# Kernel optimization log

Measured on AMD Instinct MI355X. Metric: run time of the kernel, lower is better.

The kernel has to match this reference:

```python
import jax, jax.numpy as jnp
import numpy as np

N_HEAD = 16


def setup_inputs() -> dict:
    key = jax.random.key(0)
    k1, k2, k3 = jax.random.split(key, 3)
    B, T, C = 4, 2048, 2048
    x = jax.random.normal(k1, (B, T, C), dtype=jnp.float32)
    # weights stored as [in, out] so y = x @ W + b (equivalent to torch Linear)
    w_attn = jax.random.normal(k2, (C, 3 * C), dtype=jnp.float32) * 0.02
    b_attn = jnp.zeros((3 * C,), dtype=jnp.float32)
    w_proj = jax.random.normal(k3, (C, C), dtype=jnp.float32) * 0.02
    b_proj = jnp.zeros((C,), dtype=jnp.float32)
    return {"x": x, "w_attn": w_attn, "b_attn": b_attn, "w_proj": w_proj, "b_proj": b_proj}


def reference(x, w_attn, b_attn, w_proj, b_proj):
    B, T, C = x.shape
    H = N_HEAD
    D = C // H
    qkv = x @ w_attn + b_attn                     # [B,T,3C]
    q, k, v = jnp.split(qkv, 3, axis=-1)
    q = q.reshape(B, T, H, D).transpose(0, 2, 1, 3)  # [B,H,T,D]
    k = k.reshape(B, T, H, D).transpose(0, 2, 1, 3)
    v = v.reshape(B, T, H, D).transpose(0, 2, 1, 3)
    att = jnp.einsum("bhqd,bhkd->bhqk", q, k) * (1.0 / jnp.sqrt(jnp.float32(D)))
    causal = jnp.tril(jnp.ones((T, T), dtype=bool))
    att = jnp.where(causal[None, None], att, jnp.float32(-jnp.inf))
    att = jax.nn.softmax(att, axis=-1)
    y = jnp.einsum("bhqk,bhkd->bhqd", att, v)     # [B,H,T,D]
    y = y.transpose(0, 2, 1, 3).reshape(B, T, C)
    return y @ w_proj + b_proj
```

## Files before the change

kernel.cpp:

```cpp
#include <hip/hip_runtime.h>
#include <cstdint>

typedef unsigned short u16;
typedef u16   u16x4 __attribute__((ext_vector_type(4)));
typedef u16   u16x8 __attribute__((ext_vector_type(8)));
typedef short s16x8 __attribute__((ext_vector_type(8)));
typedef float f32x4 __attribute__((ext_vector_type(4)));

__device__ __forceinline__ u16 f2bf(float f) {
  union { float f; unsigned u; } v; v.f = f;
  unsigned u = v.u;
  return (u16)((u + 0x7fffu + ((u >> 16) & 1u)) >> 16);
}

__device__ __forceinline__ void gld_lds16(const u16* g, u16* l) {
  __builtin_amdgcn_global_load_lds((const __attribute__((address_space(1))) void*)g,
                                   (__attribute__((address_space(3))) void*)l, 16, 0, 0);
}

__device__ __forceinline__ void transpose_cast_body(
    const float* __restrict__ in, u16* __restrict__ outp, int R, int Cin,
    int cx, int cy, u16 (*tile)[72]) {
  const int c0 = cx * 64, r0 = cy * 64;
  const int t = threadIdx.x;
  const int r = t >> 2, cs = (t & 3) * 16;
  const float* src = in + (size_t)(r0 + r) * Cin + c0 + cs;
#pragma unroll
  for (int q = 0; q < 4; ++q) {
    float4 v = *(const float4*)(src + q * 4);
    tile[r][cs + q * 4 + 0] = f2bf(v.x);
    tile[r][cs + q * 4 + 1] = f2bf(v.y);
    tile[r][cs + q * 4 + 2] = f2bf(v.z);
    tile[r][cs + q * 4 + 3] = f2bf(v.w);
  }
  __syncthreads();
  u16x8 w0, w1;
#pragma unroll
  for (int q = 0; q < 8; ++q) { w0[q] = tile[cs + q][r]; w1[q] = tile[cs + 8 + q][r]; }
  u16* dst = outp + (size_t)(c0 + r) * R + r0 + cs;
  *(u16x8*)dst = w0;
  *(u16x8*)(dst + 8) = w1;
}

__global__ void prep_k(const float* __restrict__ x, u16* __restrict__ xb,
                       const float* __restrict__ w_attn, u16* __restrict__ waT,
                       const float* __restrict__ w_proj, u16* __restrict__ wpT) {
  __shared__ u16 tile[64][72];
  const int bx = blockIdx.x;
  if (bx < 8192) {
    size_t i = ((size_t)bx * 256 + threadIdx.x) * 8;
    float4 a = *(const float4*)(x + i);
    float4 b = *(const float4*)(x + i + 4);
    u16x8 r;
    r[0] = f2bf(a.x); r[1] = f2bf(a.y); r[2] = f2bf(a.z); r[3] = f2bf(a.w);
    r[4] = f2bf(b.x); r[5] = f2bf(b.y); r[6] = f2bf(b.z); r[7] = f2bf(b.w);
    *(u16x8*)(xb + i) = r;
  } else if (bx < 11264) {
    int idx = bx - 8192;
    transpose_cast_body(w_attn, waT, 2048, 6144, idx % 96, idx / 96, tile);
  } else {
    int idx = bx - 11264;
    transpose_cast_body(w_proj, wpT, 2048, 2048, idx % 32, idx / 32, tile);
  }
}

template <int EPI>
__global__ __launch_bounds__(512, 2) void gemm256(
    const u16* __restrict__ A, const u16* __restrict__ Bt,
    const float* __restrict__ bias,
    u16* __restrict__ o0, u16* __restrict__ o1, u16* __restrict__ o2,
    float* __restrict__ ofp, int Ntiles, int Kdim) {
  __shared__ __align__(128) u16 sm[65536];
  const int nwg = gridDim.x;
  const int orig = blockIdx.x;
  const int qq = nwg >> 3;
  const int bid = (orig & 7) * qq + (orig >> 3);
  const int mt = bid / Ntiles, nt = bid % Ntiles;
  const int tid = threadIdx.x, lane = tid & 63, wave = tid >> 6;
  const int wr = wave >> 2, wc = wave & 3;
  const int l15 = lane & 15, lhi = lane >> 4;
  const int r7 = l15 & 7, r3 = l15 >> 3;
  f32x4 acc[8][4] = {};
  const int nK = Kdim >> 6;

#define VMA(n) asm volatile("s_waitcnt vmcnt(" #n ")" ::: "memory")
#define BARK   asm volatile("s_barrier" ::: "memory")
#define DSA(qm)                                                                          \
  do {                                                                                   \
    _Pragma("unroll") for (int mi = 0; mi < 4; ++mi)                                     \
    _Pragma("unroll") for (int kk = 0; kk < 2; ++kk)                                     \
      af[mi * 2 + kk] = *(const s16x8*)&sm[(size_t)(cA + (qm) * 1024 +                   \
          (wr * 8 + mi * 2 + r3) * 64 + r7 * 8 + (((kk) * 4 + lhi) ^ r7)) * 8];          \
  } while (0)
#define DSB(dst, qn)                                                                     \
  do {                                                                                   \
    _Pragma("unroll") for (int ni = 0; ni < 2; ++ni)                                     \
    _Pragma("unroll") for (int kk = 0; kk < 2; ++kk)                                     \
      dst[ni * 2 + kk] = *(const s16x8*)&sm[(size_t)(cB + (qn) * 1024 +                  \
          (wc * 4 + ni * 2 + r3) * 64 + r7 * 8 + (((kk) * 4 + lhi) ^ r7)) * 8];          \
  } while (0)
#define STA(unit, k0, sbase)                                                             \
  do {                                                                                   \
    _Pragma("unroll") for (int l = 0; l < 2; ++l) {                                      \
      int c = l * 512 + tid;                                                             \
      int mid = (c >> 3) & 7;                                                            \
      int rowL = (c >> 6) * 8 + mid, khi = (c & 7) ^ mid;                                \
      int prow = (rowL >> 6) * 128 + (unit) * 64 + (rowL & 63);                          \
      gld_lds16(A + (size_t)(mt * 256 + prow) * Kdim + (k0) + khi * 8,                   \
                &sm[(size_t)((sbase) + (unit)*1024 + l * 512 + wave * 64) * 8]);         \
    }                                                                                    \
  } while (0)
#define STB(unit, k0, sbase)                                                             \
  do {                                                                                   \
    _Pragma("unroll") for (int l = 0; l < 2; ++l) {                                      \
      int c = l * 512 + tid;                                                             \
      int mid = (c >> 3) & 7;                                                            \
      int colL = (c >> 6) * 8 + mid, khi = (c & 7) ^ mid;                                \
      int pcol = (colL >> 5) * 64 + (unit) * 32 + (colL & 31);                           \
      gld_lds16(Bt + (size_t)(nt * 256 + pcol) * Kdim + (k0) + khi * 8,                  \
                &sm[(size_t)((sbase) + (unit)*1024 + l * 512 + wave * 64) * 8]);         \
    }                                                                                    \
  } while (0)
#define MM(qm, qn, BF)                                                                   \
  do {                                                                                   \
    __builtin_amdgcn_s_setprio(1);                                                       \
    _Pragma("unroll") for (int mi = 0; mi < 4; ++mi)                                     \
    _Pragma("unroll") for (int ni = 0; ni < 2; ++ni)                                     \
    _Pragma("unroll") for (int kk = 0; kk < 2; ++kk)                                     \
      acc[(qm) * 4 + mi][(qn) * 2 + ni] = __builtin_amdgcn_mfma_f32_16x16x32_bf16(       \
          af[mi * 2 + kk], BF[ni * 2 + kk], acc[(qm) * 4 + mi][(qn) * 2 + ni], 0, 0, 0); \
    __builtin_amdgcn_s_setprio(0);                                                       \
  } while (0)

  STA(0, 0, 0); STB(0, 0, 4096); STB(1, 0, 4096); STA(1, 0, 0);
  VMA(4);
  BARK;

  for (int t = 0; t < nK; ++t) {
    const int cA = (t & 1) * 2048, cB = 4096 + (t & 1) * 2048;
    const int sA = ((t & 1) ^ 1) * 2048, sB = 4096 + ((t & 1) ^ 1) * 2048;
    const int k1 = (t + 1) << 6;
    const bool st = (t + 1 < nK);
    s16x8 af[8], bf0[4], bf1[4];
    DSA(0); DSB(bf0, 0);
    if (st) { STA(0, k1, sA); VMA(4); } else { VMA(2); }
    BARK; MM(0, 0, bf0); BARK;
    DSB(bf1, 1);
    if (st) { STB(0, k1, sB); VMA(4); } else { VMA(0); }
    BARK; MM(0, 1, bf1); BARK;
    DSA(1);
    if (st) STB(1, k1, sB);
    BARK; MM(1, 1, bf1); BARK;
    if (st) { STA(1, k1, sA); VMA(4); }
    BARK; MM(1, 0, bf0); BARK;
  }
#undef VMA
#undef BARK
#undef DSA
#undef DSB
#undef STA
#undef STB
#undef MM

  const int row0 = mt * 256 + wr * 128;
  const int col0 = nt * 256 + wc * 64;
  float bcol[4];
#pragma unroll
  for (int ni = 0; ni < 4; ++ni) bcol[ni] = bias[col0 + ni * 16 + l15];
  if constexpr (EPI == 0) {
#pragma unroll
    for (int ni = 0; ni < 4; ++ni) {
      int cc = col0 + ni * 16 + l15;
      int which = cc >> 11, h = (cc >> 7) & 15, d = cc & 127;
      if (which == 2) {
#pragma unroll
        for (int mi = 0; mi < 8; ++mi) {
          int t0 = row0 + mi * 16 + lhi * 4;
          int bb = t0 >> 11, tt = t0 & 2047;
          u16x4 w;
#pragma unroll
          for (int j = 0; j < 4; ++j) w[j] = f2bf(acc[mi][ni][j] + bcol[ni]);
          *(u16x4*)&o2[(((size_t)bb * 16 + h) * 128 + d) * 2048 + tt] = w;
        }
      } else {
        u16* o = (which == 0) ? o0 : o1;
#pragma unroll
        for (int mi = 0; mi < 8; ++mi)
#pragma unroll
          for (int j = 0; j < 4; ++j) {
            int row = row0 + mi * 16 + lhi * 4 + j;
            int bb = row >> 11, tt = row & 2047;
            o[(((size_t)bb * 16 + h) * 2048 + tt) * 128 + d] = f2bf(acc[mi][ni][j] + bcol[ni]);
          }
      }
    }
  } else {
#pragma unroll
    for (int mi = 0; mi < 8; ++mi)
#pragma unroll
      for (int j = 0; j < 4; ++j) {
        int row = row0 + mi * 16 + lhi * 4 + j;
#pragma unroll
        for (int ni = 0; ni < 4; ++ni)
          ofp[(size_t)row * 2048 + col0 + ni * 16 + l15] = acc[mi][ni][j] + bcol[ni];
      }
  }
}

__global__ __launch_bounds__(512, 4) void attn_k(
    const u16* __restrict__ Q, const u16* __restrict__ Kg,
    const u16* __restrict__ Vt, u16* __restrict__ Y) {
  __shared__ u16 Ks[8192];
  __shared__ u16 Vs[8192];
  __shared__ u16 Ps[8][16 * 72];
  const int p = blockIdx.x, bh = blockIdx.y;
  const int tid = threadIdx.x, lane = tid & 63, wave = tid >> 6;
  const int l15 = lane & 15, lhi = lane >> 4;
  const size_t bhT = (size_t)bh * 2048;
  const int b = bh >> 4, h = bh & 15;
  const float sc = 0.08838834764831845f * 1.4426950408889634f;

  for (int hf = 0; hf < 2; ++hf) {
    const int qt = hf ? 15 - p : p;
    const int r0 = qt * 128 + wave * 16;
    const int last = 2 * qt + 1;

    s16x8 qf[4];
#pragma unroll
    for (int kk = 0; kk < 4; ++kk)
      qf[kk] = *(const s16x8*)&Q[(bhT + r0 + l15) * 128 + kk * 32 + lhi * 8];

    f32x4 o[8] = {};
    float m_[4], l_[4];
#pragma unroll
    for (int j = 0; j < 4; ++j) { m_[j] = -1e30f; l_[j] = 0.f; }

    __syncthreads();
#pragma unroll
    for (int c = 0; c < 2; ++c) {
      int ci = c * 512 + tid;
      int dhi = ci >> 6, key = ci & 63;
      gld_lds16(Kg + (bhT + key) * 128 + dhi * 8, &Ks[(c * 512 + wave * 64) * 8]);
      int khi = ci >> 7, d = ci & 127;
      gld_lds16(Vt + ((size_t)bh * 128 + d) * 2048 + khi * 8, &Vs[(c * 512 + wave * 64) * 8]);
    }
    __syncthreads();

    for (int it = 0; it <= last; ++it) {
      const int j0 = it * 64;
      const bool have_next = (it < last);
      u16x8 kpre[2], vpre[2];
      if (have_next) {
        const int j1 = j0 + 64;
#pragma unroll
        for (int c = 0; c < 2; ++c) {
          int ci = c * 512 + tid;
          int dhi = ci >> 6, key = ci & 63;
          kpre[c] = *(const u16x8*)&Kg[(bhT + j1 + key) * 128 + dhi * 8];
          int khi = ci >> 7, d = ci & 127;
          vpre[c] = *(const u16x8*)&Vt[((size_t)bh * 128 + d) * 2048 + j1 + khi * 8];
        }
      }

      if (j0 <= r0 + 15) {
        f32x4 s[4] = {};
        __builtin_amdgcn_s_setprio(1);
#pragma unroll
        for (int nc = 0; nc < 4; ++nc)
#pragma unroll
          for (int kk = 0; kk < 4; ++kk) {
            s16x8 kf = *(const s16x8*)&Ks[((kk * 4 + lhi) * 64 + nc * 16 + l15) * 8];
            s[nc] = __builtin_amdgcn_mfma_f32_16x16x32_bf16(qf[kk], kf, s[nc], 0, 0, 0);
          }
        __builtin_amdgcn_s_setprio(0);
        const bool maskt = (j0 + 63 > r0);
        float rmax[4];
#pragma unroll
        for (int j = 0; j < 4; ++j) rmax[j] = -1e30f;
#pragma unroll
        for (int nc = 0; nc < 4; ++nc)
#pragma unroll
          for (int j = 0; j < 4; ++j) {
            float v = s[nc][j] * sc;
            if (maskt && (j0 + nc * 16 + l15) > (r0 + lhi * 4 + j)) v = -1e30f;
            s[nc][j] = v;
            rmax[j] = fmaxf(rmax[j], v);
          }
#pragma unroll
        for (int off = 1; off < 16; off <<= 1)
#pragma unroll
          for (int j = 0; j < 4; ++j) rmax[j] = fmaxf(rmax[j], __shfl_xor(rmax[j], off));

        bool up = false;
#pragma unroll
        for (int j = 0; j < 4; ++j) up |= (rmax[j] > m_[j] + 8.f);
        if (__any(up)) {
#pragma unroll
          for (int j = 0; j < 4; ++j) {
            float mn = fmaxf(m_[j], rmax[j]);
            float al = exp2f(m_[j] - mn);
            m_[j] = mn;
            l_[j] *= al;
#pragma unroll
            for (int di = 0; di < 8; ++di) o[di][j] *= al;
          }
        }
        float rsum[4];
#pragma unroll
        for (int j = 0; j < 4; ++j) rsum[j] = 0.f;
#pragma unroll
        for (int nc = 0; nc < 4; ++nc)
#pragma unroll
          for (int j = 0; j < 4; ++j) {
            float pv = exp2f(s[nc][j] - m_[j]);
            rsum[j] += pv;
            Ps[wave][(lhi * 4 + j) * 72 + nc * 16 + l15] = f2bf(pv);
          }
#pragma unroll
        for (int off = 1; off < 16; off <<= 1)
#pragma unroll
          for (int j = 0; j < 4; ++j) rsum[j] += __shfl_xor(rsum[j], off);
#pragma unroll
        for (int j = 0; j < 4; ++j) l_[j] += rsum[j];

        __builtin_amdgcn_s_setprio(1);
#pragma unroll
        for (int kk2 = 0; kk2 < 2; ++kk2) {
          s16x8 pf = *(const s16x8*)&Ps[wave][l15 * 72 + kk2 * 32 + lhi * 8];
#pragma unroll
          for (int di = 0; di < 8; ++di) {
            s16x8 vf = *(const s16x8*)&Vs[((kk2 * 4 + lhi) * 128 + di * 16 + l15) * 8];
            o[di] = __builtin_amdgcn_mfma_f32_16x16x32_bf16(pf, vf, o[di], 0, 0, 0);
          }
        }
        __builtin_amdgcn_s_setprio(0);
      }

      if (have_next) {
        __syncthreads();
#pragma unroll
        for (int c = 0; c < 2; ++c) {
          *(u16x8*)&Ks[(c * 512 + tid) * 8] = kpre[c];
          *(u16x8*)&Vs[(c * 512 + tid) * 8] = vpre[c];
        }
        __syncthreads();
      }
    }

    float rl[4];
#pragma unroll
    for (int j = 0; j < 4; ++j) rl[j] = 1.0f / l_[j];
#pragma unroll
    for (int di = 0; di < 8; ++di)
#pragma unroll
      for (int j = 0; j < 4; ++j) {
        int row = b * 2048 + r0 + lhi * 4 + j;
        int col = h * 128 + di * 16 + l15;
        Y[(size_t)row * 2048 + col] = f2bf(o[di][j] * rl[j]);
      }
  }
}

extern "C" void kernel_launch(void* const* d_in, const int* in_sizes, int n_in,
                              void* d_out, int out_size, void* d_ws, size_t ws_size,
                              hipStream_t stream) {
  const float* x      = (const float*)d_in[0];
  const float* w_attn = (const float*)d_in[1];
  const float* b_attn = (const float*)d_in[2];
  const float* w_proj = (const float*)d_in[3];
  const float* b_proj = (const float*)d_in[4];
  float* out = (float*)d_out;

  char* ws = (char*)d_ws;
  u16* xb  = (u16*)(ws);
  u16* waT = (u16*)(ws + 33554432ull);
  u16* wpT = (u16*)(ws + 58720256ull);
  u16* Qb  = (u16*)(ws + 67108864ull);
  u16* Kb  = (u16*)(ws + 100663296ull);
  u16* Vtb = (u16*)(ws + 167772160ull);
  u16* Yb  = xb;

  prep_k<<<12288, 256, 0, stream>>>(x, xb, w_attn, waT, w_proj, wpT);
  gemm256<0><<<32 * 24, 512, 0, stream>>>(xb, waT, b_attn, Qb, Kb, Vtb, nullptr, 24, 2048);
  attn_k<<<dim3(8, 64), 512, 0, stream>>>(Qb, Kb, Vtb, Yb);
  gemm256<1><<<32 * 8, 512, 0, stream>>>(Yb, wpT, b_proj, nullptr, nullptr, nullptr, out, 8, 2048);
}
```

Measured before the change: 487.2 us.

## Double-buffer attention K/V tiles in LDS with async global-to-LDS loads

The attention kernel now keeps two LDS buffers for K and V. Each iteration issues direct global-to-LDS loads for the next tile into the spare buffer while computing on the current one. This replaces the register prefetch and its two barriers plus LDS stores with a single barrier per iteration, and aims to hide load latency and cut register pressure. The grid axes are also swapped so head/batch varies fastest, which changes block scheduling order. In exchange, LDS use per block roughly doubles for K/V, which may lower the number of resident blocks per CU.

After: 525.6 us. +7.9%, slower.

```diff
diff --git a/kernel.cpp b/kernel.cpp
--- a/kernel.cpp
+++ b/kernel.cpp
@@ -210,16 +210,30 @@
 __global__ __launch_bounds__(512, 4) void attn_k(
     const u16* __restrict__ Q, const u16* __restrict__ Kg,
     const u16* __restrict__ Vt, u16* __restrict__ Y) {
-  __shared__ u16 Ks[8192];
-  __shared__ u16 Vs[8192];
+  __shared__ u16 Ks[2][8192];
+  __shared__ u16 Vs[2][8192];
   __shared__ u16 Ps[8][16 * 72];
-  const int p = blockIdx.x, bh = blockIdx.y;
+  const int bh = blockIdx.x, p = blockIdx.y;
   const int tid = threadIdx.x, lane = tid & 63, wave = tid >> 6;
   const int l15 = lane & 15, lhi = lane >> 4;
   const size_t bhT = (size_t)bh * 2048;
   const int b = bh >> 4, h = bh & 15;
   const float sc = 0.08838834764831845f * 1.4426950408889634f;
 
+#define STAGEKV(buf, jt)                                                   \
+  do {                                                                     \
+    const int jb_ = (jt) * 64;                                             \
+    _Pragma("unroll") for (int c = 0; c < 2; ++c) {                        \
+      int ci = c * 512 + tid;                                              \
+      int dhi = ci >> 6, key = ci & 63;                                    \
+      gld_lds16(Kg + (bhT + jb_ + key) * 128 + dhi * 8,                    \
+                &Ks[buf][(c * 512 + wave * 64) * 8]);                      \
+      int khi = ci >> 7, d = ci & 127;                                     \
+      gld_lds16(Vt + ((size_t)bh * 128 + d) * 2048 + jb_ + khi * 8,        \
+                &Vs[buf][(c * 512 + wave * 64) * 8]);                      \
+    }                                                                      \
+  } while (0)
+
   for (int hf = 0; hf < 2; ++hf) {
     const int qt = hf ? 15 - p : p;
     const int r0 = qt * 128 + wave * 16;
@@ -236,31 +250,13 @@
     for (int j = 0; j < 4; ++j) { m_[j] = -1e30f; l_[j] = 0.f; }
 
     __syncthreads();
-#pragma unroll
-    for (int c = 0; c < 2; ++c) {
-      int ci = c * 512 + tid;
-      int dhi = ci >> 6, key = ci & 63;
-      gld_lds16(Kg + (bhT + key) * 128 + dhi * 8, &Ks[(c * 512 + wave * 64) * 8]);
-      int khi = ci >> 7, d = ci & 127;
-      gld_lds16(Vt + ((size_t)bh * 128 + d) * 2048 + khi * 8, &Vs[(c * 512 + wave * 64) * 8]);
-    }
-    __syncthreads();
+    STAGEKV(0, 0);
 
     for (int it = 0; it <= last; ++it) {
       const int j0 = it * 64;
-      const bool have_next = (it < last);
-      u16x8 kpre[2], vpre[2];
-      if (have_next) {
-        const int j1 = j0 + 64;
-#pragma unroll
-        for (int c = 0; c < 2; ++c) {
-          int ci = c * 512 + tid;
-          int dhi = ci >> 6, key = ci & 63;
-          kpre[c] = *(const u16x8*)&Kg[(bhT + j1 + key) * 128 + dhi * 8];
-          int khi = ci >> 7, d = ci & 127;
-          vpre[c] = *(const u16x8*)&Vt[((size_t)bh * 128 + d) * 2048 + j1 + khi * 8];
-        }
-      }
+      const int buf = it & 1;
+      __syncthreads();
+      if (it < last) STAGEKV(buf ^ 1, it + 1);
 
       if (j0 <= r0 + 15) {
         f32x4 s[4] = {};
@@ -269,7 +265,7 @@
         for (int nc = 0; nc < 4; ++nc)
 #pragma unroll
           for (int kk = 0; kk < 4; ++kk) {
-            s16x8 kf = *(const s16x8*)&Ks[((kk * 4 + lhi) * 64 + nc * 16 + l15) * 8];
+            s16x8 kf = *(const s16x8*)&Ks[buf][((kk * 4 + lhi) * 64 + nc * 16 + l15) * 8];
             s[nc] = __builtin_amdgcn_mfma_f32_16x16x32_bf16(qf[kk], kf, s[nc], 0, 0, 0);
           }
         __builtin_amdgcn_s_setprio(0);
@@ -329,21 +325,11 @@
           s16x8 pf = *(const s16x8*)&Ps[wave][l15 * 72 + kk2 * 32 + lhi * 8];
 #pragma unroll
           for (int di = 0; di < 8; ++di) {
-            s16x8 vf = *(const s16x8*)&Vs[((kk2 * 4 + lhi) * 128 + di * 16 + l15) * 8];
+            s16x8 vf = *(const s16x8*)&Vs[buf][((kk2 * 4 + lhi) * 128 + di * 16 + l15) * 8];
             o[di] = __builtin_amdgcn_mfma_f32_16x16x32_bf16(pf, vf, o[di], 0, 0, 0);
           }
         }
         __builtin_amdgcn_s_setprio(0);
-      }
-
-      if (have_next) {
-        __syncthreads();
-#pragma unroll
-        for (int c = 0; c < 2; ++c) {
-          *(u16x8*)&Ks[(c * 512 + tid) * 8] = kpre[c];
-          *(u16x8*)&Vs[(c * 512 + tid) * 8] = vpre[c];
-        }
-        __syncthreads();
       }
     }
 
@@ -359,6 +345,7 @@
         Y[(size_t)row * 2048 + col] = f2bf(o[di][j] * rl[j]);
       }
   }
+#undef STAGEKV
 }
 
 extern "C" void kernel_launch(void* const* d_in, const int* in_sizes, int n_in,
@@ -382,6 +369,6 @@
 
   prep_k<<<12288, 256, 0, stream>>>(x, xb, w_attn, waT, w_proj, wpT);
   gemm256<0><<<32 * 24, 512, 0, stream>>>(xb, waT, b_attn, Qb, Kb, Vtb, nullptr, 24, 2048);
-  attn_k<<<dim3(8, 64), 512, 0, stream>>>(Qb, Kb, Vtb, Yb);
+  attn_k<<<dim3(64, 8), 512, 0, stream>>>(Qb, Kb, Vtb, Yb);
   gemm256<1><<<32 * 8, 512, 0, stream>>>(Yb, wpT, b_proj, nullptr, nullptr, nullptr, out, 8, 2048);
 }
```
